# Kernel optimization log

Measured on AMD Instinct MI355X. Metric: run time of the kernel, lower is better.

## Reference

```python
import jax, jax.numpy as jnp
import numpy as np

PH, PW, PS = 4, 4, 16          # patch grid h/w and patch_size
SEQ = PS * PS                  # 256 tokens per chunk
EH = EW = ET = 4               # mem_expand_size
RPW = 2 * EW + 1               # 9
RPH = 2 * EH + 1               # 9
RPF = RPH * RPW                # 81
HEADS, DHEAD, DIM = 16, 64, 1024
INNER = HEADS * DHEAD
SCALE = DHEAD ** -0.5


def _pos(idx):
    nf = PH * PW
    inner = idx % nf
    return inner % PH, inner // PH, idx // nf


def _rotary(freqs, t):
    # freqs: [n, rot_dim] broadcast over leading dims of t [..., n, rot_dim]
    x1 = t[..., 0::2]
    x2 = t[..., 1::2]
    rot = jnp.stack((-x2, x1), axis=-1).reshape(t.shape)
    return t * jnp.cos(freqs) + rot * jnp.sin(freqs)


def setup_inputs() -> dict:
    key = jax.random.key(0)
    ks = jax.random.split(key, 9)
    B, M, TXT = 16, 8, 77
    KV = M * SEQ + TXT
    return {
        "x": jax.random.normal(ks[0], (B, SEQ, DIM), jnp.float32),
        "cond": jax.random.normal(ks[1], (B, KV, DIM), jnp.float32),
        "freqs": jax.random.normal(ks[2], (PH * PS, PW * PS, DHEAD), jnp.float32),
        "Wq": jax.random.normal(ks[3], (DIM, INNER), jnp.float32) * 0.02,
        "Wk": jax.random.normal(ks[4], (DIM, INNER), jnp.float32) * 0.02,
        "Wv": jax.random.normal(ks[5], (DIM, INNER), jnp.float32) * 0.02,
        "rel_table": jax.random.normal(ks[6], (RPH * RPW * (2 * ET + 1), HEADS), jnp.float32) * 0.02,
        "Wo": jax.random.normal(ks[7], (INNER, DIM), jnp.float32) * 0.02,
        "bo": jax.random.normal(ks[8], (DIM,), jnp.float32) * 0.02,
        "mem_idxs": jnp.arange(8, dtype=jnp.int64) if jax.config.jax_enable_x64 else jnp.arange(8, dtype=jnp.int32),
        "cur_patch_idx": 21,
    }


def reference(x, cond, freqs, Wq, Wk, Wv, rel_table, Wo, bo, mem_idxs, cur_patch_idx):
    B = x.shape[0]
    M = mem_idxs.shape[0]
    MS = M * SEQ
    # QKV projections -> [b, h, n, d]
    q = (x @ Wq).reshape(B, SEQ, HEADS, DHEAD).transpose(0, 2, 1, 3)
    k = (cond @ Wk).reshape(B, -1, HEADS, DHEAD).transpose(0, 2, 1, 3)
    v = (cond @ Wv).reshape(B, -1, HEADS, DHEAD).transpose(0, 2, 1, 3)

    # relative position indices (gather into bias table)
    rs, cs, ts = _pos(cur_patch_idx)           # python ints (static)
    rt, ct, tt = _pos(mem_idxs)                # [M] arrays
    rel_idx = (rt - rs + EH) * RPW + (ct - cs + EW) + (tt - ts + ET) * RPF
    bias = rel_table[rel_idx]                  # [M, H]
    bias = jnp.repeat(bias.T, SEQ, axis=1)[None, :, :, None]  # [1, H, M*SEQ, 1]
    km = k[:, :, :MS] + bias                   # bias added to memory K before rotary

    # rotary freqs: source patch (static slice) and target patches (gathered)
    src = freqs[rs * PS:(rs + 1) * PS, cs * PS:(cs + 1) * PS].reshape(SEQ, -1)
    rows = rt[:, None] * PS + jnp.arange(PS)   # [M, PS]
    cols = ct[:, None] * PS + jnp.arange(PS)   # [M, PS]
    tgt = freqs[rows[:, :, None], cols[:, None, :]].reshape(MS, -1)  # [M*SEQ, rot]

    q = _rotary(src, q)
    km = _rotary(tgt, km)
    k = jnp.concatenate([km, k[:, :, MS:]], axis=2)

    dots = jnp.einsum('bhid,bhjd->bhij', q, k) * SCALE
    attn = jax.nn.softmax(dots, axis=-1)
    out = jnp.einsum('bhij,bhjd->bhid', attn, v)
    out = out.transpose(0, 2, 1, 3).reshape(B, SEQ, INNER)
    return out @ Wo + bo
```

## Files before the change

### kernel.cpp

```cpp
#include <hip/hip_runtime.h>
#include <cstdint>

typedef __bf16 bf16;
typedef bf16 bf16x2 __attribute__((ext_vector_type(2)));
typedef bf16 bf16x4 __attribute__((ext_vector_type(4)));
typedef bf16 bf16x8 __attribute__((ext_vector_type(8)));
typedef float floatx4 __attribute__((ext_vector_type(4)));

#define SEQ   256
#define DIMM  1024
#define HEADS 16
#define KV_LEN 2125
#define KV_PAD 2176
#define KV_BLKS 17
#define MS_TOK 2048
#define ATT_SCALE 0.125f
#define TILE_ELEMS (128 * 32)

__device__ __forceinline__ void load_lds16(const bf16* g, bf16* l) {
    __builtin_amdgcn_global_load_lds(
        (const __attribute__((address_space(1))) void*)g,
        (__attribute__((address_space(3))) void*)l, 16, 0, 0);
}

__global__ __launch_bounds__(256) void convert_kernel(
        const float* __restrict__ src, bf16* __restrict__ dst, long total) {
    long i4 = ((long)blockIdx.x * 256 + threadIdx.x) * 4;
    if (i4 >= total) return;
    const float4 v = *(const float4*)(src + i4);
    bf16x4 o;
    o[0] = (bf16)v.x; o[1] = (bf16)v.y; o[2] = (bf16)v.z; o[3] = (bf16)v.w;
    *(bf16x4*)(dst + i4) = o;
}

__global__ __launch_bounds__(256) void convert_cond_kernel(
        const float* __restrict__ src, bf16* __restrict__ dst, long total_dst) {
    long i4 = ((long)blockIdx.x * 256 + threadIdx.x) * 4;
    if (i4 >= total_dst) return;
    long drow = i4 >> 10;
    int b = (int)(drow / KV_PAD);
    int j = (int)(drow - (long)b * KV_PAD);
    bf16x4 o;
    if (j < KV_LEN) {
        long srow = (long)b * KV_LEN + j;
        const float4 v = *(const float4*)(src + (srow << 10) + (i4 & 1023));
        o[0] = (bf16)v.x; o[1] = (bf16)v.y; o[2] = (bf16)v.z; o[3] = (bf16)v.w;
    } else {
        o[0] = o[1] = o[2] = o[3] = (bf16)0.f;
    }
    *(bf16x4*)(dst + i4) = o;
}

__global__ __launch_bounds__(256) void transpose_bf16_kernel(
        const float* __restrict__ W, bf16* __restrict__ Wt, int N) {
    __shared__ float tile[32][33];
    int n0 = blockIdx.x * 32, k0 = blockIdx.y * 32;
    int r = threadIdx.x >> 5, c = threadIdx.x & 31;
    #pragma unroll
    for (int i = 0; i < 4; ++i)
        tile[r + i * 8][c] = W[(size_t)(k0 + r + i * 8) * N + n0 + c];
    __syncthreads();
    #pragma unroll
    for (int i = 0; i < 4; ++i)
        Wt[(size_t)(n0 + r + i * 8) * N + k0 + c] = (bf16)tile[c][r + i * 8];
}

__global__ __launch_bounds__(256) void rot_tables_kernel(
        const float* __restrict__ freqs, const float* __restrict__ rel_table,
        const int* __restrict__ mem_idxs, const int* __restrict__ cur,
        float* __restrict__ ckT, float* __restrict__ skT,
        float* __restrict__ cqT, float* __restrict__ sqT,
        float* __restrict__ biasK) {
    int t = blockIdx.x * 256 + threadIdx.x;
    const int cp = *cur; const int inner = cp & 15;
    const int rs = inner & 3, cs = inner >> 2, ts = cp >> 4;
    if (t < MS_TOK * 64) {
        int j = t >> 6, d = t & 63;
        int mi = mem_idxs[j >> 8];
        int rt = mi & 3, ct = (mi >> 2) & 3;
        int pidx = j & 255;
        int fr = rt * 16 + (pidx >> 4), fc = ct * 16 + (pidx & 15);
        float f = freqs[(size_t)(fr * 64 + fc) * 64 + d];
        ckT[t] = __cosf(f); skT[t] = __sinf(f);
    } else if (t < MS_TOK * 64 + SEQ * 64) {
        int t2 = t - MS_TOK * 64;
        int s = t2 >> 6, d = t2 & 63;
        int fr = rs * 16 + (s >> 4), fc = cs * 16 + (s & 15);
        float f = freqs[(size_t)(fr * 64 + fc) * 64 + d];
        cqT[t2] = __cosf(f); sqT[t2] = __sinf(f);
    } else if (t < MS_TOK * 64 + SEQ * 64 + 128) {
        int t3 = t - (MS_TOK * 64 + SEQ * 64);
        int m = t3 >> 4, h = t3 & 15;
        int mi = mem_idxs[m];
        int rt = mi & 3, ct = (mi >> 2) & 3, tt = mi >> 4;
        int rel = (rt - rs + 4) * 9 + (ct - cs + 4) + (tt - ts + 4) * 81;
        biasK[t3] = rel_table[rel * HEADS + h];
    }
}

__device__ __forceinline__ void gemm_loop_db(
        const bf16* __restrict__ Ag, const bf16* __restrict__ Bg, int K,
        bf16* __restrict__ As, bf16* __restrict__ Bs,
        floatx4 (&acc)[4][4]) {
    const int tid  = threadIdx.x;
    const int wave = tid >> 6, lane = tid & 63;
    const int quad = lane >> 4, l16 = lane & 15;
    const int wm = wave >> 1, wn = wave & 1;
    #pragma unroll
    for (int i = 0; i < 2; ++i) {
        int c = i * 256 + wave * 64 + lane;
        int r = c >> 2, c8 = (c & 3) * 8;
        load_lds16(Ag + (long)r * K + c8, As + (i * 256 + wave * 64) * 8);
        load_lds16(Bg + (long)r * K + c8, Bs + (i * 256 + wave * 64) * 8);
    }
    for (int k0 = 0; k0 < K; k0 += 32) {
        const int cur = (k0 >> 5) & 1;
        bf16* Asc = As + cur * TILE_ELEMS;
        bf16* Bsc = Bs + cur * TILE_ELEMS;
        __syncthreads();
        if (k0 + 32 < K) {
            bf16* Asn = As + (cur ^ 1) * TILE_ELEMS;
            bf16* Bsn = Bs + (cur ^ 1) * TILE_ELEMS;
            #pragma unroll
            for (int i = 0; i < 2; ++i) {
                int c = i * 256 + wave * 64 + lane;
                int r = c >> 2, c8 = (c & 3) * 8;
                load_lds16(Ag + (long)r * K + k0 + 32 + c8, Asn + (i * 256 + wave * 64) * 8);
                load_lds16(Bg + (long)r * K + k0 + 32 + c8, Bsn + (i * 256 + wave * 64) * 8);
            }
        }
        bf16x8 af[4], bfr[4];
        #pragma unroll
        for (int mt = 0; mt < 4; ++mt)
            af[mt] = *(const bf16x8*)(Asc + (wm * 64 + mt * 16 + l16) * 32 + quad * 8);
        #pragma unroll
        for (int nt = 0; nt < 4; ++nt)
            bfr[nt] = *(const bf16x8*)(Bsc + (wn * 64 + nt * 16 + l16) * 32 + quad * 8);
        #pragma unroll
        for (int mt = 0; mt < 4; ++mt)
            #pragma unroll
            for (int nt = 0; nt < 4; ++nt)
                acc[mt][nt] = __builtin_amdgcn_mfma_f32_16x16x32_bf16(af[mt], bfr[nt], acc[mt][nt], 0, 0, 0);
    }
}

__global__ __launch_bounds__(256) void gemm_o_kernel(
        const bf16* __restrict__ A, const bf16* __restrict__ Bt,
        float* __restrict__ Cout, const float* __restrict__ bias, int N) {
    __shared__ bf16 As[2 * TILE_ELEMS];
    __shared__ bf16 Bs[2 * TILE_ELEMS];
    const int tid  = threadIdx.x;
    const int wave = tid >> 6, lane = tid & 63;
    const int quad = lane >> 4, l16 = lane & 15;
    const int wm = wave >> 1, wn = wave & 1;
    const int L = blockIdx.x, xcd = L & 7, ii = L >> 3;
    const long row0 = (long)(xcd * 4 + (ii >> 3)) * 128;
    const long col0 = (long)(ii & 7) * 128;
    floatx4 acc[4][4] = {};
    gemm_loop_db(A + row0 * DIMM, Bt + col0 * DIMM, DIMM, As, Bs, acc);
    #pragma unroll
    for (int mt = 0; mt < 4; ++mt) {
        #pragma unroll
        for (int nt = 0; nt < 4; ++nt) {
            long r = row0 + wm * 64 + mt * 16 + quad * 4;
            long ccol = col0 + wn * 64 + nt * 16 + l16;
            float bv = bias[ccol];
            #pragma unroll
            for (int i = 0; i < 4; ++i)
                Cout[(r + i) * (long)N + ccol] = acc[mt][nt][i] + bv;
        }
    }
}

__global__ __launch_bounds__(256) void gemm_q_rot_kernel(
        const bf16* __restrict__ A, const bf16* __restrict__ Bt,
        bf16* __restrict__ Qout, const float* __restrict__ cqT,
        const float* __restrict__ sqT) {
    __shared__ bf16 As[2 * TILE_ELEMS];
    __shared__ bf16 Bs[2 * TILE_ELEMS];
    const int tid  = threadIdx.x;
    const int wave = tid >> 6, lane = tid & 63;
    const int quad = lane >> 4, l16 = lane & 15;
    const int wm = wave >> 1, wn = wave & 1;
    const int L = blockIdx.x, xcd = L & 7, ii = L >> 3;
    const long row0 = (long)(xcd * 4 + (ii >> 3)) * 128;
    const long col0 = (long)(ii & 7) * 128;
    floatx4 acc[4][4] = {};
    gemm_loop_db(A + row0 * DIMM, Bt + col0 * DIMM, DIMM, As, Bs, acc);
    #pragma unroll
    for (int mt = 0; mt < 4; ++mt) {
        #pragma unroll
        for (int nt = 0; nt < 4; ++nt) {
            long rr = row0 + wm * 64 + mt * 16 + quad * 4;
            int ccol = (int)col0 + wn * 64 + nt * 16 + l16;
            int d = ccol & 63;
            #pragma unroll
            for (int i = 0; i < 4; ++i) {
                long r = rr + i; int s = (int)(r & 255);
                float c_ = cqT[s * 64 + d], s_ = sqT[s * 64 + d];
                float q = acc[mt][nt][i];
                float pn = __shfl_xor(q, 1);
                float outv = (d & 1) ? (q * c_ + pn * s_) : (q * c_ - pn * s_);
                Qout[r * DIMM + ccol] = (bf16)outv;
            }
        }
    }
}

__global__ __launch_bounds__(256) void gemm_k_kernel(
        const bf16* __restrict__ A, const bf16* __restrict__ Btk,
        bf16* __restrict__ Kout, const float* __restrict__ ckT,
        const float* __restrict__ skT, const float* __restrict__ biasK) {
    __shared__ bf16 As[2 * TILE_ELEMS];
    __shared__ bf16 Bs[2 * TILE_ELEMS];
    const int tid  = threadIdx.x;
    const int wave = tid >> 6, lane = tid & 63;
    const int quad = lane >> 4, l16 = lane & 15;
    const int wm = wave >> 1, wn = wave & 1;
    const int L = blockIdx.x, xcd = L & 7, ii = L >> 3;
    const long row0 = (long)(xcd * 34 + (ii >> 3)) * 128;
    const long col0 = (long)(ii & 7) * 128;
    floatx4 acc[4][4] = {};
    gemm_loop_db(A + row0 * DIMM, Btk + col0 * DIMM, DIMM, As, Bs, acc);
    const int bidx = (int)(row0 / KV_PAD);
    #pragma unroll
    for (int mt = 0; mt < 4; ++mt) {
        #pragma unroll
        for (int nt = 0; nt < 4; ++nt) {
            long rr = row0 + wm * 64 + mt * 16 + quad * 4;
            int ccol = (int)col0 + wn * 64 + nt * 16 + l16;
            int h = ccol >> 6, d = ccol & 63;
            int jbase = (int)(rr - (long)bidx * KV_PAD);
            #pragma unroll
            for (int i = 0; i < 4; ++i) {
                int j = jbase + i;
                float kb = acc[mt][nt][i];
                float c_ = 1.f, s_ = 0.f;
                if (j < MS_TOK) {
                    kb += biasK[((j >> 8) << 4) + h];
                    c_ = ckT[j * 64 + d]; s_ = skT[j * 64 + d];
                }
                float pn = __shfl_xor(kb, 1);
                float outv = (d & 1) ? (kb * c_ + pn * s_) : (kb * c_ - pn * s_);
                Kout[(rr + i) * DIMM + ccol] = (bf16)outv;
            }
        }
    }
}

__global__ __launch_bounds__(256) void gemm_vt_kernel(
        const bf16* __restrict__ Wvt, const bf16* __restrict__ condb,
        bf16* __restrict__ VT) {
    __shared__ bf16 As[2 * TILE_ELEMS];
    __shared__ bf16 Bs[2 * TILE_ELEMS];
    const int tid  = threadIdx.x;
    const int wave = tid >> 6, lane = tid & 63;
    const int quad = lane >> 4, l16 = lane & 15;
    const int wm = wave >> 1, wn = wave & 1;
    const int L = blockIdx.x, xcd = L & 7, ii = L >> 3;
    const int pan = xcd * 34 + (ii >> 3);
    const int b  = pan / KV_BLKS, tb = pan % KV_BLKS;
    const long row0 = (long)(ii & 7) * 128;
    const long col0 = (long)tb * 128;
    const bf16* Bt = condb + (size_t)b * KV_PAD * DIMM;
    floatx4 acc[4][4] = {};
    gemm_loop_db(Wvt + row0 * DIMM, Bt + col0 * DIMM, DIMM, As, Bs, acc);
    #pragma unroll
    for (int mt = 0; mt < 4; ++mt) {
        #pragma unroll
        for (int nt = 0; nt < 4; ++nt) {
            long f0 = row0 + wm * 64 + mt * 16 + quad * 4;
            long t0 = col0 + wn * 64 + nt * 16 + l16;
            #pragma unroll
            for (int i = 0; i < 4; ++i)
                VT[((size_t)b * DIMM + f0 + i) * KV_PAD + t0] = (bf16)acc[mt][nt][i];
        }
    }
}

__global__ __launch_bounds__(256, 3) void attn_kernel(
        const bf16* __restrict__ Qb, const bf16* __restrict__ Kb,
        const bf16* __restrict__ VT, bf16* __restrict__ Ob) {
    const int L = blockIdx.x, xcd = L & 7, ii = L >> 3;
    const int bh = xcd * 32 + (ii >> 2), qt = ii & 3;
    const int b = bh >> 4, h = bh & 15;
    const int tid = threadIdx.x, wave = tid >> 6, lane = tid & 63;
    const int quad = lane >> 4, l16 = lane & 15;
    __shared__ bf16 Ks[128 * 72];
    __shared__ bf16 Vt[64 * 144];
    __shared__ bf16 Ps[4][16 * 72];

    const int qrow0 = b * SEQ + qt * 64 + wave * 16;
    const bf16* qp = Qb + (size_t)(qrow0 + l16) * DIMM + h * 64 + quad * 8;
    bf16x8 qf0 = *(const bf16x8*)(qp);
    bf16x8 qf1 = *(const bf16x8*)(qp + 32);

    floatx4 oacc[4] = {};
    floatx4 lacc = {};
    bf16x8 ones;
    #pragma unroll
    for (int t = 0; t < 8; ++t) ones[t] = (bf16)1.0f;

    const size_t kbase = ((size_t)b * KV_PAD) * DIMM + h * 64;
    const size_t vbase = ((size_t)(bh * 64)) * KV_PAD;

    const int kchunk = tid & 1;
    const int gl = tid >> 1;
    const int g  = ((gl & 31) << 2) | (gl >> 5);
    const int gg = g & 63;
    const int dstrow = (g >> 6) * 64 + ((gg & 3) << 4) + (gg >> 2);
    const int vd = tid >> 2, vseg = tid & 3;

    bf16x8 kr[4], vr[4];
    {
        int jr = g; if (jr > KV_LEN - 1) jr = KV_LEN - 1;
        const bf16* gp = Kb + kbase + (size_t)jr * DIMM + kchunk * 32;
        kr[0] = *(const bf16x8*)(gp);      kr[1] = *(const bf16x8*)(gp + 8);
        kr[2] = *(const bf16x8*)(gp + 16); kr[3] = *(const bf16x8*)(gp + 24);
        const bf16* vp = VT + vbase + (size_t)vd * KV_PAD + vseg * 32;
        vr[0] = *(const bf16x8*)(vp);      vr[1] = *(const bf16x8*)(vp + 8);
        vr[2] = *(const bf16x8*)(vp + 16); vr[3] = *(const bf16x8*)(vp + 24);
    }

    for (int j0 = 0; j0 < KV_LEN; j0 += 128) {
        __syncthreads();
        {
            bf16* dp = Ks + dstrow * 72 + kchunk * 32;
            *(bf16x8*)(dp)      = kr[0]; *(bf16x8*)(dp + 8)  = kr[1];
            *(bf16x8*)(dp + 16) = kr[2]; *(bf16x8*)(dp + 24) = kr[3];
            bf16* dv = Vt + vd * 144 + vseg * 32;
            *(bf16x8*)(dv)      = vr[0]; *(bf16x8*)(dv + 8)  = vr[1];
            *(bf16x8*)(dv + 16) = vr[2]; *(bf16x8*)(dv + 24) = vr[3];
        }
        __syncthreads();
        if (j0 + 128 < KV_LEN) {
            int jr = j0 + 128 + g; if (jr > KV_LEN - 1) jr = KV_LEN - 1;
            const bf16* gp = Kb + kbase + (size_t)jr * DIMM + kchunk * 32;
            kr[0] = *(const bf16x8*)(gp);      kr[1] = *(const bf16x8*)(gp + 8);
            kr[2] = *(const bf16x8*)(gp + 16); kr[3] = *(const bf16x8*)(gp + 24);
            const bf16* vp = VT + vbase + (size_t)vd * KV_PAD + j0 + 128 + vseg * 32;
            vr[0] = *(const bf16x8*)(vp);      vr[1] = *(const bf16x8*)(vp + 8);
            vr[2] = *(const bf16x8*)(vp + 16); vr[3] = *(const bf16x8*)(vp + 24);
        }
        #pragma unroll
        for (int c = 0; c < 2; ++c) {
            floatx4 s[4] = {};
            #pragma unroll
            for (int jt = 0; jt < 4; ++jt) {
                const bf16* kp = Ks + (c * 64 + jt * 16 + l16) * 72 + quad * 8;
                bf16x8 kb0 = *(const bf16x8*)(kp);
                bf16x8 kb1 = *(const bf16x8*)(kp + 32);
                s[jt] = __builtin_amdgcn_mfma_f32_16x16x32_bf16(qf0, kb0, s[jt], 0, 0, 0);
                s[jt] = __builtin_amdgcn_mfma_f32_16x16x32_bf16(qf1, kb1, s[jt], 0, 0, 0);
            }
            const int colbase = j0 + c * 64 + 4 * l16;
            #pragma unroll
            for (int r = 0; r < 4; ++r) {
                bf16x4 pk;
                #pragma unroll
                for (int jt = 0; jt < 4; ++jt) {
                    bool ok = (colbase + jt) < KV_LEN;
                    float p = ok ? __expf(s[jt][r] * ATT_SCALE) : 0.f;
                    pk[jt] = (bf16)p;
                }
                *(bf16x4*)(&Ps[wave][(quad * 4 + r) * 72 + l16 * 4]) = pk;
            }
            #pragma unroll
            for (int kf = 0; kf < 2; ++kf) {
                bf16x8 pa = *(const bf16x8*)(&Ps[wave][l16 * 72 + kf * 32 + quad * 8]);
                lacc = __builtin_amdgcn_mfma_f32_16x16x32_bf16(pa, ones, lacc, 0, 0, 0);
                #pragma unroll
                for (int dt = 0; dt < 4; ++dt) {
                    bf16x8 vb = *(const bf16x8*)(Vt + (dt * 16 + l16) * 144 + c * 64 + kf * 32 + quad * 8);
                    oacc[dt] = __builtin_amdgcn_mfma_f32_16x16x32_bf16(pa, vb, oacc[dt], 0, 0, 0);
                }
            }
        }
    }
    #pragma unroll
    for (int r = 0; r < 4; ++r) {
        float inv = 1.f / lacc[r];
        size_t orow = (size_t)(qrow0 + quad * 4 + r) * DIMM + h * 64;
        #pragma unroll
        for (int dt = 0; dt < 4; ++dt)
            Ob[orow + dt * 16 + l16] = (bf16)(oacc[dt][r] * inv);
    }
}

extern "C" void kernel_launch(void* const* d_in, const int* in_sizes, int n_in,
                              void* d_out, int out_size, void* d_ws, size_t ws_size,
                              hipStream_t stream) {
    const float* x     = (const float*)d_in[0];
    const float* cond  = (const float*)d_in[1];
    const float* freqs = (const float*)d_in[2];
    const float* Wq    = (const float*)d_in[3];
    const float* Wk    = (const float*)d_in[4];
    const float* Wv    = (const float*)d_in[5];
    const float* rel   = (const float*)d_in[6];
    const float* Wo    = (const float*)d_in[7];
    const float* bo    = (const float*)d_in[8];
    const int* mem_idxs = (const int*)d_in[9];
    const int* cur      = (const int*)d_in[10];
    float* out = (float*)d_out;

    const int B   = 16;
    const int Mq  = B * SEQ;
    const int Mkv_pad = B * KV_PAD;

    char* ws = (char*)d_ws;
    size_t off = 0;
    auto alloc = [&](size_t bytes) { void* pp = ws + off; off = (off + bytes + 255) & ~(size_t)255; return pp; };
    bf16* xb    = (bf16*)alloc((size_t)Mq * DIMM * 2);
    bf16* condb = (bf16*)alloc((size_t)Mkv_pad * DIMM * 2);
    bf16* Wqt   = (bf16*)alloc((size_t)DIMM * DIMM * 2);
    bf16* Wkt   = (bf16*)alloc((size_t)DIMM * DIMM * 2);
    bf16* Wvt   = (bf16*)alloc((size_t)DIMM * DIMM * 2);
    bf16* Wot   = (bf16*)alloc((size_t)DIMM * DIMM * 2);
    bf16* Qb    = (bf16*)alloc((size_t)Mq * DIMM * 2);
    bf16* Kb    = (bf16*)alloc((size_t)Mkv_pad * DIMM * 2);
    bf16* VTb   = (bf16*)alloc((size_t)B * DIMM * KV_PAD * 2);
    bf16* Ab    = (bf16*)alloc((size_t)Mq * DIMM * 2);
    float* ckT  = (float*)alloc((size_t)MS_TOK * 64 * 4);
    float* skT  = (float*)alloc((size_t)MS_TOK * 64 * 4);
    float* cqT  = (float*)alloc((size_t)SEQ * 64 * 4);
    float* sqT  = (float*)alloc((size_t)SEQ * 64 * 4);
    float* biasK = (float*)alloc(128 * 4);

    long xtot = (long)Mq * DIMM;
    convert_kernel<<<(int)((xtot / 4 + 255) / 256), 256, 0, stream>>>(x, xb, xtot);
    long ctot = (long)Mkv_pad * DIMM;
    convert_cond_kernel<<<(int)((ctot / 4 + 255) / 256), 256, 0, stream>>>(cond, condb, ctot);
    dim3 tg(32, 32);
    transpose_bf16_kernel<<<tg, 256, 0, stream>>>(Wq, Wqt, DIMM);
    transpose_bf16_kernel<<<tg, 256, 0, stream>>>(Wk, Wkt, DIMM);
    transpose_bf16_kernel<<<tg, 256, 0, stream>>>(Wv, Wvt, DIMM);
    transpose_bf16_kernel<<<tg, 256, 0, stream>>>(Wo, Wot, DIMM);

    int ttot = MS_TOK * 64 + SEQ * 64 + 128;
    rot_tables_kernel<<<(ttot + 255) / 256, 256, 0, stream>>>(
        freqs, rel, mem_idxs, cur, ckT, skT, cqT, sqT, biasK);

    gemm_q_rot_kernel<<<256, 256, 0, stream>>>(xb, Wqt, Qb, cqT, sqT);
    gemm_k_kernel<<<2176, 256, 0, stream>>>(condb, Wkt, Kb, ckT, skT, biasK);
    gemm_vt_kernel<<<2176, 256, 0, stream>>>(Wvt, condb, VTb);

    attn_kernel<<<1024, 256, 0, stream>>>(Qb, Kb, VTb, Ab);

    gemm_o_kernel<<<256, 256, 0, stream>>>(Ab, Wot, out, bo, DIMM);
}
```

Baseline: 590.3 us.

## Fuse K and V projection GEMMs into one kernel sharing the cond tile

Merges the separate K-projection and transposed-V-projection GEMMs into a single kernel that loads each cond tile once and multiplies it against both Wk and Wv, keeping two accumulator sets. V is written transposed using packed 4-element stores. This drops one full pass over cond and one kernel launch. In exchange it doubles the accumulator registers and adds LDS buffering, which may reduce occupancy.

```diff
diff --git a/kernel.cpp b/kernel.cpp
--- a/kernel.cpp
+++ b/kernel.cpp
@@ -207,12 +207,14 @@
     }
 }
 
-__global__ __launch_bounds__(256) void gemm_k_kernel(
+__global__ __launch_bounds__(256) void gemm_kv_kernel(
         const bf16* __restrict__ A, const bf16* __restrict__ Btk,
-        bf16* __restrict__ Kout, const float* __restrict__ ckT,
+        const bf16* __restrict__ Btv, bf16* __restrict__ Kout,
+        bf16* __restrict__ VT, const float* __restrict__ ckT,
         const float* __restrict__ skT, const float* __restrict__ biasK) {
     __shared__ bf16 As[2 * TILE_ELEMS];
-    __shared__ bf16 Bs[2 * TILE_ELEMS];
+    __shared__ bf16 Bks[2 * TILE_ELEMS];
+    __shared__ bf16 Bvs[2 * TILE_ELEMS];
     const int tid  = threadIdx.x;
     const int wave = tid >> 6, lane = tid & 63;
     const int quad = lane >> 4, l16 = lane & 15;
@@ -220,9 +222,62 @@
     const int L = blockIdx.x, xcd = L & 7, ii = L >> 3;
     const long row0 = (long)(xcd * 34 + (ii >> 3)) * 128;
     const long col0 = (long)(ii & 7) * 128;
-    floatx4 acc[4][4] = {};
-    gemm_loop_db(A + row0 * DIMM, Btk + col0 * DIMM, DIMM, As, Bs, acc);
+    const bf16* Ag  = A   + row0 * DIMM;
+    const bf16* Bkg = Btk + col0 * DIMM;
+    const bf16* Bvg = Btv + col0 * DIMM;
+
+    floatx4 acck[4][4] = {};
+    floatx4 accv[4][4] = {};
+
+    #pragma unroll
+    for (int i = 0; i < 2; ++i) {
+        int c = i * 256 + wave * 64 + lane;
+        int r = c >> 2, c8 = (c & 3) * 8;
+        int du = (i * 256 + wave * 64) * 8;
+        load_lds16(Ag  + (long)r * DIMM + c8, As  + du);
+        load_lds16(Bkg + (long)r * DIMM + c8, Bks + du);
+        load_lds16(Bvg + (long)r * DIMM + c8, Bvs + du);
+    }
+    for (int k0 = 0; k0 < DIMM; k0 += 32) {
+        const int cur = (k0 >> 5) & 1;
+        const bf16* Asc  = As  + cur * TILE_ELEMS;
+        const bf16* Bksc = Bks + cur * TILE_ELEMS;
+        const bf16* Bvsc = Bvs + cur * TILE_ELEMS;
+        __syncthreads();
+        if (k0 + 32 < DIMM) {
+            bf16* Asn  = As  + (cur ^ 1) * TILE_ELEMS;
+            bf16* Bksn = Bks + (cur ^ 1) * TILE_ELEMS;
+            bf16* Bvsn = Bvs + (cur ^ 1) * TILE_ELEMS;
+            #pragma unroll
+            for (int i = 0; i < 2; ++i) {
+                int c = i * 256 + wave * 64 + lane;
+                int r = c >> 2, c8 = (c & 3) * 8;
+                int du = (i * 256 + wave * 64) * 8;
+                load_lds16(Ag  + (long)r * DIMM + k0 + 32 + c8, Asn  + du);
+                load_lds16(Bkg + (long)r * DIMM + k0 + 32 + c8, Bksn + du);
+                load_lds16(Bvg + (long)r * DIMM + k0 + 32 + c8, Bvsn + du);
+            }
+        }
+        bf16x8 af[4], bk[4], bv[4];
+        #pragma unroll
+        for (int mt = 0; mt < 4; ++mt)
+            af[mt] = *(const bf16x8*)(Asc + (wm * 64 + mt * 16 + l16) * 32 + quad * 8);
+        #pragma unroll
+        for (int nt = 0; nt < 4; ++nt) {
+            bk[nt] = *(const bf16x8*)(Bksc + (wn * 64 + nt * 16 + l16) * 32 + quad * 8);
+            bv[nt] = *(const bf16x8*)(Bvsc + (wn * 64 + nt * 16 + l16) * 32 + quad * 8);
+        }
+        #pragma unroll
+        for (int mt = 0; mt < 4; ++mt)
+            #pragma unroll
+            for (int nt = 0; nt < 4; ++nt) {
+                acck[mt][nt] = __builtin_amdgcn_mfma_f32_16x16x32_bf16(af[mt], bk[nt], acck[mt][nt], 0, 0, 0);
+                accv[mt][nt] = __builtin_amdgcn_mfma_f32_16x16x32_bf16(af[mt], bv[nt], accv[mt][nt], 0, 0, 0);
+            }
+    }
+
     const int bidx = (int)(row0 / KV_PAD);
+    const int jpan = (int)(row0 - (long)bidx * KV_PAD);
     #pragma unroll
     for (int mt = 0; mt < 4; ++mt) {
         #pragma unroll
@@ -230,11 +285,11 @@
             long rr = row0 + wm * 64 + mt * 16 + quad * 4;
             int ccol = (int)col0 + wn * 64 + nt * 16 + l16;
             int h = ccol >> 6, d = ccol & 63;
-            int jbase = (int)(rr - (long)bidx * KV_PAD);
+            int jbase = jpan + wm * 64 + mt * 16 + quad * 4;
             #pragma unroll
             for (int i = 0; i < 4; ++i) {
                 int j = jbase + i;
-                float kb = acc[mt][nt][i];
+                float kb = acck[mt][nt][i];
                 float c_ = 1.f, s_ = 0.f;
                 if (j < MS_TOK) {
                     kb += biasK[((j >> 8) << 4) + h];
@@ -246,34 +301,16 @@
             }
         }
     }
-}
-
-__global__ __launch_bounds__(256) void gemm_vt_kernel(
-        const bf16* __restrict__ Wvt, const bf16* __restrict__ condb,
-        bf16* __restrict__ VT) {
-    __shared__ bf16 As[2 * TILE_ELEMS];
-    __shared__ bf16 Bs[2 * TILE_ELEMS];
-    const int tid  = threadIdx.x;
-    const int wave = tid >> 6, lane = tid & 63;
-    const int quad = lane >> 4, l16 = lane & 15;
-    const int wm = wave >> 1, wn = wave & 1;
-    const int L = blockIdx.x, xcd = L & 7, ii = L >> 3;
-    const int pan = xcd * 34 + (ii >> 3);
-    const int b  = pan / KV_BLKS, tb = pan % KV_BLKS;
-    const long row0 = (long)(ii & 7) * 128;
-    const long col0 = (long)tb * 128;
-    const bf16* Bt = condb + (size_t)b * KV_PAD * DIMM;
-    floatx4 acc[4][4] = {};
-    gemm_loop_db(Wvt + row0 * DIMM, Bt + col0 * DIMM, DIMM, As, Bs, acc);
     #pragma unroll
     for (int mt = 0; mt < 4; ++mt) {
+        int jv = jpan + wm * 64 + mt * 16 + quad * 4;
         #pragma unroll
         for (int nt = 0; nt < 4; ++nt) {
-            long f0 = row0 + wm * 64 + mt * 16 + quad * 4;
-            long t0 = col0 + wn * 64 + nt * 16 + l16;
-            #pragma unroll
-            for (int i = 0; i < 4; ++i)
-                VT[((size_t)b * DIMM + f0 + i) * KV_PAD + t0] = (bf16)acc[mt][nt][i];
+            int f = (int)col0 + wn * 64 + nt * 16 + l16;
+            bf16x4 pk;
+            #pragma unroll
+            for (int i = 0; i < 4; ++i) pk[i] = (bf16)accv[mt][nt][i];
+            *(bf16x4*)(&VT[((size_t)bidx * DIMM + f) * KV_PAD + jv]) = pk;
         }
     }
 }
@@ -441,8 +478,7 @@
         freqs, rel, mem_idxs, cur, ckT, skT, cqT, sqT, biasK);
 
     gemm_q_rot_kernel<<<256, 256, 0, stream>>>(xb, Wqt, Qb, cqT, sqT);
-    gemm_k_kernel<<<2176, 256, 0, stream>>>(condb, Wkt, Kb, ckT, skT, biasK);
-    gemm_vt_kernel<<<2176, 256, 0, stream>>>(Wvt, condb, VTb);
+    gemm_kv_kernel<<<2176, 256, 0, stream>>>(condb, Wkt, Wvt, Kb, VTb, ckT, skT, biasK);
 
     attn_kernel<<<1024, 256, 0, stream>>>(Qb, Kb, VTb, Ab);
 
```

Result: slower. 791.4 us (+34.1%).

## Merge Q/K/V projection GEMMs into one launch; attention handles 128 query rows per block

Applied to the files above, without the earlier changes.

The three projection GEMMs (K with bias and rotary, V transposed, Q with rotary) now run as one grid that dispatches on block index, which removes two launch gaps and lets the tail of one GEMM overlap with the next. The attention kernel now gives each block 128 query rows, two 64-row sub-tiles per wave, so every K/V tile staged in LDS is reused twice and the grid halves to 512 blocks. The larger accumulator state raises register pressure, so the occupancy hint drops from 3 to 2 blocks per CU, and the smaller grid may leave some CUs underused.

```diff
diff --git a/kernel.cpp b/kernel.cpp
--- a/kernel.cpp
+++ b/kernel.cpp
@@ -16,6 +16,10 @@
 #define MS_TOK 2048
 #define ATT_SCALE 0.125f
 #define TILE_ELEMS (128 * 32)
+
+#define G3_K   2176
+#define G3_VT  (G3_K + 2176)
+#define G3_END (G3_VT + 256)
 
 __device__ __forceinline__ void load_lds16(const bf16* g, bf16* l) {
     __builtin_amdgcn_global_load_lds(
@@ -144,6 +148,99 @@
     }
 }
 
+__global__ __launch_bounds__(256) void gemm3_kernel(
+        const bf16* __restrict__ xb, const bf16* __restrict__ condb,
+        const bf16* __restrict__ Wqt, const bf16* __restrict__ Wkt,
+        const bf16* __restrict__ Wvt,
+        bf16* __restrict__ Qb, bf16* __restrict__ Kout, bf16* __restrict__ VT,
+        const float* __restrict__ cqT, const float* __restrict__ sqT,
+        const float* __restrict__ ckT, const float* __restrict__ skT,
+        const float* __restrict__ biasK) {
+    __shared__ bf16 As[2 * TILE_ELEMS];
+    __shared__ bf16 Bs[2 * TILE_ELEMS];
+    const int tid  = threadIdx.x;
+    const int wave = tid >> 6, lane = tid & 63;
+    const int quad = lane >> 4, l16 = lane & 15;
+    const int wm = wave >> 1, wn = wave & 1;
+    const int Lb = blockIdx.x;
+
+    if (Lb < G3_K) {
+        const int L = Lb, xcd = L & 7, ii = L >> 3;
+        const long row0 = (long)(xcd * 34 + (ii >> 3)) * 128;
+        const long col0 = (long)(ii & 7) * 128;
+        floatx4 acc[4][4] = {};
+        gemm_loop_db(condb + row0 * DIMM, Wkt + col0 * DIMM, DIMM, As, Bs, acc);
+        const int bidx = (int)(row0 / KV_PAD);
+        #pragma unroll
+        for (int mt = 0; mt < 4; ++mt) {
+            #pragma unroll
+            for (int nt = 0; nt < 4; ++nt) {
+                long rr = row0 + wm * 64 + mt * 16 + quad * 4;
+                int ccol = (int)col0 + wn * 64 + nt * 16 + l16;
+                int h = ccol >> 6, d = ccol & 63;
+                int jbase = (int)(rr - (long)bidx * KV_PAD);
+                #pragma unroll
+                for (int i = 0; i < 4; ++i) {
+                    int j = jbase + i;
+                    float kb = acc[mt][nt][i];
+                    float c_ = 1.f, s_ = 0.f;
+                    if (j < MS_TOK) {
+                        kb += biasK[((j >> 8) << 4) + h];
+                        c_ = ckT[j * 64 + d]; s_ = skT[j * 64 + d];
+                    }
+                    float pn = __shfl_xor(kb, 1);
+                    float outv = (d & 1) ? (kb * c_ + pn * s_) : (kb * c_ - pn * s_);
+                    Kout[(rr + i) * DIMM + ccol] = (bf16)outv;
+                }
+            }
+        }
+    } else if (Lb < G3_VT) {
+        const int L = Lb - G3_K, xcd = L & 7, ii = L >> 3;
+        const int pan = xcd * 34 + (ii >> 3);
+        const int b  = pan / KV_BLKS, tb = pan % KV_BLKS;
+        const long row0 = (long)(ii & 7) * 128;
+        const long col0 = (long)tb * 128;
+        const bf16* Bt = condb + (size_t)b * KV_PAD * DIMM;
+        floatx4 acc[4][4] = {};
+        gemm_loop_db(Wvt + row0 * DIMM, Bt + col0 * DIMM, DIMM, As, Bs, acc);
+        #pragma unroll
+        for (int mt = 0; mt < 4; ++mt) {
+            #pragma unroll
+            for (int nt = 0; nt < 4; ++nt) {
+                long f0 = row0 + wm * 64 + mt * 16 + quad * 4;
+                long t0 = col0 + wn * 64 + nt * 16 + l16;
+                #pragma unroll
+                for (int i = 0; i < 4; ++i)
+                    VT[((size_t)b * DIMM + f0 + i) * KV_PAD + t0] = (bf16)acc[mt][nt][i];
+            }
+        }
+    } else {
+        const int L = Lb - G3_VT, xcd = L & 7, ii = L >> 3;
+        const long row0 = (long)(xcd * 4 + (ii >> 3)) * 128;
+        const long col0 = (long)(ii & 7) * 128;
+        floatx4 acc[4][4] = {};
+        gemm_loop_db(xb + row0 * DIMM, Wqt + col0 * DIMM, DIMM, As, Bs, acc);
+        #pragma unroll
+        for (int mt = 0; mt < 4; ++mt) {
+            #pragma unroll
+            for (int nt = 0; nt < 4; ++nt) {
+                long rr = row0 + wm * 64 + mt * 16 + quad * 4;
+                int ccol = (int)col0 + wn * 64 + nt * 16 + l16;
+                int d = ccol & 63;
+                #pragma unroll
+                for (int i = 0; i < 4; ++i) {
+                    long r = rr + i; int s = (int)(r & 255);
+                    float c_ = cqT[s * 64 + d], s_ = sqT[s * 64 + d];
+                    float q = acc[mt][nt][i];
+                    float pn = __shfl_xor(q, 1);
+                    float outv = (d & 1) ? (q * c_ + pn * s_) : (q * c_ - pn * s_);
+                    Qb[r * DIMM + ccol] = (bf16)outv;
+                }
+            }
+        }
+    }
+}
+
 __global__ __launch_bounds__(256) void gemm_o_kernel(
         const bf16* __restrict__ A, const bf16* __restrict__ Bt,
         float* __restrict__ Cout, const float* __restrict__ bias, int N) {
@@ -172,117 +269,11 @@
     }
 }
 
-__global__ __launch_bounds__(256) void gemm_q_rot_kernel(
-        const bf16* __restrict__ A, const bf16* __restrict__ Bt,
-        bf16* __restrict__ Qout, const float* __restrict__ cqT,
-        const float* __restrict__ sqT) {
-    __shared__ bf16 As[2 * TILE_ELEMS];
-    __shared__ bf16 Bs[2 * TILE_ELEMS];
-    const int tid  = threadIdx.x;
-    const int wave = tid >> 6, lane = tid & 63;
-    const int quad = lane >> 4, l16 = lane & 15;
-    const int wm = wave >> 1, wn = wave & 1;
-    const int L = blockIdx.x, xcd = L & 7, ii = L >> 3;
-    const long row0 = (long)(xcd * 4 + (ii >> 3)) * 128;
-    const long col0 = (long)(ii & 7) * 128;
-    floatx4 acc[4][4] = {};
-    gemm_loop_db(A + row0 * DIMM, Bt + col0 * DIMM, DIMM, As, Bs, acc);
-    #pragma unroll
-    for (int mt = 0; mt < 4; ++mt) {
-        #pragma unroll
-        for (int nt = 0; nt < 4; ++nt) {
-            long rr = row0 + wm * 64 + mt * 16 + quad * 4;
-            int ccol = (int)col0 + wn * 64 + nt * 16 + l16;
-            int d = ccol & 63;
-            #pragma unroll
-            for (int i = 0; i < 4; ++i) {
-                long r = rr + i; int s = (int)(r & 255);
-                float c_ = cqT[s * 64 + d], s_ = sqT[s * 64 + d];
-                float q = acc[mt][nt][i];
-                float pn = __shfl_xor(q, 1);
-                float outv = (d & 1) ? (q * c_ + pn * s_) : (q * c_ - pn * s_);
-                Qout[r * DIMM + ccol] = (bf16)outv;
-            }
-        }
-    }
-}
-
-__global__ __launch_bounds__(256) void gemm_k_kernel(
-        const bf16* __restrict__ A, const bf16* __restrict__ Btk,
-        bf16* __restrict__ Kout, const float* __restrict__ ckT,
-        const float* __restrict__ skT, const float* __restrict__ biasK) {
-    __shared__ bf16 As[2 * TILE_ELEMS];
-    __shared__ bf16 Bs[2 * TILE_ELEMS];
-    const int tid  = threadIdx.x;
-    const int wave = tid >> 6, lane = tid & 63;
-    const int quad = lane >> 4, l16 = lane & 15;
-    const int wm = wave >> 1, wn = wave & 1;
-    const int L = blockIdx.x, xcd = L & 7, ii = L >> 3;
-    const long row0 = (long)(xcd * 34 + (ii >> 3)) * 128;
-    const long col0 = (long)(ii & 7) * 128;
-    floatx4 acc[4][4] = {};
-    gemm_loop_db(A + row0 * DIMM, Btk + col0 * DIMM, DIMM, As, Bs, acc);
-    const int bidx = (int)(row0 / KV_PAD);
-    #pragma unroll
-    for (int mt = 0; mt < 4; ++mt) {
-        #pragma unroll
-        for (int nt = 0; nt < 4; ++nt) {
-            long rr = row0 + wm * 64 + mt * 16 + quad * 4;
-            int ccol = (int)col0 + wn * 64 + nt * 16 + l16;
-            int h = ccol >> 6, d = ccol & 63;
-            int jbase = (int)(rr - (long)bidx * KV_PAD);
-            #pragma unroll
-            for (int i = 0; i < 4; ++i) {
-                int j = jbase + i;
-                float kb = acc[mt][nt][i];
-                float c_ = 1.f, s_ = 0.f;
-                if (j < MS_TOK) {
-                    kb += biasK[((j >> 8) << 4) + h];
-                    c_ = ckT[j * 64 + d]; s_ = skT[j * 64 + d];
-                }
-                float pn = __shfl_xor(kb, 1);
-                float outv = (d & 1) ? (kb * c_ + pn * s_) : (kb * c_ - pn * s_);
-                Kout[(rr + i) * DIMM + ccol] = (bf16)outv;
-            }
-        }
-    }
-}
-
-__global__ __launch_bounds__(256) void gemm_vt_kernel(
-        const bf16* __restrict__ Wvt, const bf16* __restrict__ condb,
-        bf16* __restrict__ VT) {
-    __shared__ bf16 As[2 * TILE_ELEMS];
-    __shared__ bf16 Bs[2 * TILE_ELEMS];
-    const int tid  = threadIdx.x;
-    const int wave = tid >> 6, lane = tid & 63;
-    const int quad = lane >> 4, l16 = lane & 15;
-    const int wm = wave >> 1, wn = wave & 1;
-    const int L = blockIdx.x, xcd = L & 7, ii = L >> 3;
-    const int pan = xcd * 34 + (ii >> 3);
-    const int b  = pan / KV_BLKS, tb = pan % KV_BLKS;
-    const long row0 = (long)(ii & 7) * 128;
-    const long col0 = (long)tb * 128;
-    const bf16* Bt = condb + (size_t)b * KV_PAD * DIMM;
-    floatx4 acc[4][4] = {};
-    gemm_loop_db(Wvt + row0 * DIMM, Bt + col0 * DIMM, DIMM, As, Bs, acc);
-    #pragma unroll
-    for (int mt = 0; mt < 4; ++mt) {
-        #pragma unroll
-        for (int nt = 0; nt < 4; ++nt) {
-            long f0 = row0 + wm * 64 + mt * 16 + quad * 4;
-            long t0 = col0 + wn * 64 + nt * 16 + l16;
-            #pragma unroll
-            for (int i = 0; i < 4; ++i)
-                VT[((size_t)b * DIMM + f0 + i) * KV_PAD + t0] = (bf16)acc[mt][nt][i];
-        }
-    }
-}
-
-__global__ __launch_bounds__(256, 3) void attn_kernel(
+__global__ __launch_bounds__(256, 2) void attn_kernel(
         const bf16* __restrict__ Qb, const bf16* __restrict__ Kb,
         const bf16* __restrict__ VT, bf16* __restrict__ Ob) {
     const int L = blockIdx.x, xcd = L & 7, ii = L >> 3;
-    const int bh = xcd * 32 + (ii >> 2), qt = ii & 3;
+    const int bh = xcd * 32 + (ii >> 1), half = ii & 1;
     const int b = bh >> 4, h = bh & 15;
     const int tid = threadIdx.x, wave = tid >> 6, lane = tid & 63;
     const int quad = lane >> 4, l16 = lane & 15;
@@ -290,13 +281,17 @@
     __shared__ bf16 Vt[64 * 144];
     __shared__ bf16 Ps[4][16 * 72];
 
-    const int qrow0 = b * SEQ + qt * 64 + wave * 16;
-    const bf16* qp = Qb + (size_t)(qrow0 + l16) * DIMM + h * 64 + quad * 8;
-    bf16x8 qf0 = *(const bf16x8*)(qp);
-    bf16x8 qf1 = *(const bf16x8*)(qp + 32);
-
-    floatx4 oacc[4] = {};
-    floatx4 lacc = {};
+    const int qrow0 = b * SEQ + half * 128 + wave * 16;
+    bf16x8 qf0[2], qf1[2];
+    #pragma unroll
+    for (int qs = 0; qs < 2; ++qs) {
+        const bf16* qp = Qb + (size_t)(qrow0 + qs * 64 + l16) * DIMM + h * 64 + quad * 8;
+        qf0[qs] = *(const bf16x8*)(qp);
+        qf1[qs] = *(const bf16x8*)(qp + 32);
+    }
+
+    floatx4 oacc[2][4] = {};
+    floatx4 lacc[2] = {};
     bf16x8 ones;
     #pragma unroll
     for (int t = 0; t < 8; ++t) ones[t] = (bf16)1.0f;
@@ -344,14 +339,16 @@
         }
         #pragma unroll
         for (int c = 0; c < 2; ++c) {
-            floatx4 s[4] = {};
+            floatx4 sa[4] = {}, sb[4] = {};
             #pragma unroll
             for (int jt = 0; jt < 4; ++jt) {
                 const bf16* kp = Ks + (c * 64 + jt * 16 + l16) * 72 + quad * 8;
                 bf16x8 kb0 = *(const bf16x8*)(kp);
                 bf16x8 kb1 = *(const bf16x8*)(kp + 32);
-                s[jt] = __builtin_amdgcn_mfma_f32_16x16x32_bf16(qf0, kb0, s[jt], 0, 0, 0);
-                s[jt] = __builtin_amdgcn_mfma_f32_16x16x32_bf16(qf1, kb1, s[jt], 0, 0, 0);
+                sa[jt] = __builtin_amdgcn_mfma_f32_16x16x32_bf16(qf0[0], kb0, sa[jt], 0, 0, 0);
+                sa[jt] = __builtin_amdgcn_mfma_f32_16x16x32_bf16(qf1[0], kb1, sa[jt], 0, 0, 0);
+                sb[jt] = __builtin_amdgcn_mfma_f32_16x16x32_bf16(qf0[1], kb0, sb[jt], 0, 0, 0);
+                sb[jt] = __builtin_amdgcn_mfma_f32_16x16x32_bf16(qf1[1], kb1, sb[jt], 0, 0, 0);
             }
             const int colbase = j0 + c * 64 + 4 * l16;
             #pragma unroll
@@ -360,7 +357,7 @@
                 #pragma unroll
                 for (int jt = 0; jt < 4; ++jt) {
                     bool ok = (colbase + jt) < KV_LEN;
-                    float p = ok ? __expf(s[jt][r] * ATT_SCALE) : 0.f;
+                    float p = ok ? __expf(sa[jt][r] * ATT_SCALE) : 0.f;
                     pk[jt] = (bf16)p;
                 }
                 *(bf16x4*)(&Ps[wave][(quad * 4 + r) * 72 + l16 * 4]) = pk;
@@ -368,22 +365,46 @@
             #pragma unroll
             for (int kf = 0; kf < 2; ++kf) {
                 bf16x8 pa = *(const bf16x8*)(&Ps[wave][l16 * 72 + kf * 32 + quad * 8]);
-                lacc = __builtin_amdgcn_mfma_f32_16x16x32_bf16(pa, ones, lacc, 0, 0, 0);
+                lacc[0] = __builtin_amdgcn_mfma_f32_16x16x32_bf16(pa, ones, lacc[0], 0, 0, 0);
                 #pragma unroll
                 for (int dt = 0; dt < 4; ++dt) {
                     bf16x8 vb = *(const bf16x8*)(Vt + (dt * 16 + l16) * 144 + c * 64 + kf * 32 + quad * 8);
-                    oacc[dt] = __builtin_amdgcn_mfma_f32_16x16x32_bf16(pa, vb, oacc[dt], 0, 0, 0);
-                }
-            }
-        }
-    }
-    #pragma unroll
-    for (int r = 0; r < 4; ++r) {
-        float inv = 1.f / lacc[r];
-        size_t orow = (size_t)(qrow0 + quad * 4 + r) * DIMM + h * 64;
-        #pragma unroll
-        for (int dt = 0; dt < 4; ++dt)
-            Ob[orow + dt * 16 + l16] = (bf16)(oacc[dt][r] * inv);
+                    oacc[0][dt] = __builtin_amdgcn_mfma_f32_16x16x32_bf16(pa, vb, oacc[0][dt], 0, 0, 0);
+                }
+            }
+            #pragma unroll
+            for (int r = 0; r < 4; ++r) {
+                bf16x4 pk;
+                #pragma unroll
+                for (int jt = 0; jt < 4; ++jt) {
+                    bool ok = (colbase + jt) < KV_LEN;
+                    float p = ok ? __expf(sb[jt][r] * ATT_SCALE) : 0.f;
+                    pk[jt] = (bf16)p;
+                }
+                *(bf16x4*)(&Ps[wave][(quad * 4 + r) * 72 + l16 * 4]) = pk;
+            }
+            #pragma unroll
+            for (int kf = 0; kf < 2; ++kf) {
+                bf16x8 pa = *(const bf16x8*)(&Ps[wave][l16 * 72 + kf * 32 + quad * 8]);
+                lacc[1] = __builtin_amdgcn_mfma_f32_16x16x32_bf16(pa, ones, lacc[1], 0, 0, 0);
+                #pragma unroll
+                for (int dt = 0; dt < 4; ++dt) {
+                    bf16x8 vb = *(const bf16x8*)(Vt + (dt * 16 + l16) * 144 + c * 64 + kf * 32 + quad * 8);
+                    oacc[1][dt] = __builtin_amdgcn_mfma_f32_16x16x32_bf16(pa, vb, oacc[1][dt], 0, 0, 0);
+                }
+            }
+        }
+    }
+    #pragma unroll
+    for (int qs = 0; qs < 2; ++qs) {
+        #pragma unroll
+        for (int r = 0; r < 4; ++r) {
+            float inv = 1.f / lacc[qs][r];
+            size_t orow = (size_t)(qrow0 + qs * 64 + quad * 4 + r) * DIMM + h * 64;
+            #pragma unroll
+            for (int dt = 0; dt < 4; ++dt)
+                Ob[orow + dt * 16 + l16] = (bf16)(oacc[qs][dt][r] * inv);
+        }
     }
 }
 
@@ -440,11 +461,10 @@
     rot_tables_kernel<<<(ttot + 255) / 256, 256, 0, stream>>>(
         freqs, rel, mem_idxs, cur, ckT, skT, cqT, sqT, biasK);
 
-    gemm_q_rot_kernel<<<256, 256, 0, stream>>>(xb, Wqt, Qb, cqT, sqT);
-    gemm_k_kernel<<<2176, 256, 0, stream>>>(condb, Wkt, Kb, ckT, skT, biasK);
-    gemm_vt_kernel<<<2176, 256, 0, stream>>>(Wvt, condb, VTb);
-
-    attn_kernel<<<1024, 256, 0, stream>>>(Qb, Kb, VTb, Ab);
+    gemm3_kernel<<<G3_END, 256, 0, stream>>>(
+        xb, condb, Wqt, Wkt, Wvt, Qb, Kb, VTb, cqT, sqT, ckT, skT, biasK);
+
+    attn_kernel<<<512, 256, 0, stream>>>(Qb, Kb, VTb, Ab);
 
     gemm_o_kernel<<<256, 256, 0, stream>>>(Ab, Wot, out, bo, DIMM);
 }
```

Result: slower. 614.6 us (+4.1%).
